# Kernel tuning notes

Hardware: AMD Instinct MI355X
Metric: run time of the kernel (lower is better)

## Reference

```python
import jax, jax.numpy as jnp
import numpy as np

B, T, D, DFF = 8, 2048, 1024, 4096
EPS = 1e-6
PLIF_ALPHA = 2.0


@jax.custom_vjp
def spike_fn(m):
    # hard threshold forward, atan surrogate backward (PLIF neuron)
    return (m > 0.0).astype(m.dtype)

def _spk_fwd(m):
    return (m > 0.0).astype(m.dtype), m

def _spk_bwd(m, g):
    ds = PLIF_ALPHA / (2.0 * (1.0 + (jnp.pi * 0.5 * PLIF_ALPHA * m) ** 2))
    return (g * ds,)

spike_fn.defvjp(_spk_fwd, _spk_bwd)


def _rmsnorm(x, w):
    rstd = jax.lax.rsqrt(jnp.mean(x * x, axis=-1, keepdims=True) + EPS)
    return x * rstd * w


def setup_inputs() -> dict:
    key = jax.random.key(0)
    ks = jax.random.split(key, 9)
    sc = 0.02
    return {
        'x': jax.random.normal(ks[0], (B, T, D), jnp.float32),
        'rms_w1': jnp.ones((D,), jnp.float32),
        'rms_w2': jnp.ones((D,), jnp.float32),
        'delta_w': sc * jax.random.normal(ks[1], (D, D), jnp.float32),
        'delta_b': jnp.zeros((D,), jnp.float32),
        'b_w': sc * jax.random.normal(ks[2], (D, D), jnp.float32),
        'b_b': jnp.zeros((D,), jnp.float32),
        'A_log': jnp.log(jnp.linspace(0.5, 2.0, D).astype(jnp.float32)),
        'log_tau': jnp.full((D,), jnp.log(2.0), jnp.float32),
        'plif_thr': jnp.ones((D,), jnp.float32),
        'syn_w': sc * jax.random.normal(ks[3], (D, D), jnp.float32),
        'syn_b': jnp.zeros((D,), jnp.float32),
        'gate_w': sc * jax.random.normal(ks[4], (D, D), jnp.float32),
        'gate_b': jnp.zeros((D,), jnp.float32),
        'ffn_g_w': sc * jax.random.normal(ks[5], (DFF, D), jnp.float32),
        'ffn_u_w': sc * jax.random.normal(ks[6], (DFF, D), jnp.float32),
        'ffn_d_w': sc * jax.random.normal(ks[7], (D, DFF), jnp.float32),
    }


def _forward(x, rms_w1, rms_w2, delta_w, delta_b, b_w, b_b, A_log, log_tau,
             plif_thr, syn_w, syn_b, gate_w, gate_b, ffn_g_w, ffn_u_w, ffn_d_w):
    Bx, Tx, Dx = x.shape
    # --- RMSNorm 1 ---
    y1 = _rmsnorm(x, rms_w1)
    # --- selective-scan style liquid inputs ---
    delta = jax.nn.softplus(jnp.einsum('btd,ed->bte', y1, delta_w) + delta_b)  # [B,T,D]
    bvec = delta * (jnp.einsum('btd,ed->bte', y1, b_w) + b_b)                  # [B,T,D]
    A = jnp.exp(-delta * jnp.exp(A_log))                                        # [B,T,D]

    # --- liquid recurrent scan: h_t = tanh(A_t * h_{t-1} + b_t) ---
    def liquid_step(h, ab):
        a_t, b_t = ab
        h = jnp.tanh(a_t * h + b_t)
        return h, h

    h0 = jnp.zeros((Bx, Dx), x.dtype)
    _, h_post = jax.lax.scan(liquid_step, h0,
                             (jnp.swapaxes(A, 0, 1), jnp.swapaxes(bvec, 0, 1)))
    h_post = jnp.swapaxes(h_post, 0, 1)  # [B,T,D]

    # --- PLIF spiking scan with soft reset ---
    pdec = jnp.exp(-1.0 / jnp.exp(log_tau))  # [D]

    def plif_step(v, h_t):
        v_pre = pdec * v + (1.0 - pdec) * h_t
        s = spike_fn(v_pre - plif_thr)
        return v_pre - s * plif_thr, s

    v0 = jnp.zeros((Bx, Dx), x.dtype)
    _, spike = jax.lax.scan(plif_step, v0, jnp.swapaxes(h_post, 0, 1))
    spike = jnp.swapaxes(spike, 0, 1)

    # --- SEW shortcut + synaptic gate ---
    spike_in = spike + h_post
    syn = jnp.einsum('btd,ed->bte', spike_in, syn_w) + syn_b
    gate = jax.nn.sigmoid(jnp.einsum('btd,ed->bte', spike_in, gate_w) + gate_b)
    x1 = x + syn * gate

    # --- RMSNorm 2 + SwiGLU FFN + residual ---
    y2 = _rmsnorm(x1, rms_w2)
    ffn_act = jax.nn.silu(y2 @ ffn_g_w.T) * (y2 @ ffn_u_w.T)
    return x1 + ffn_act @ ffn_d_w.T


def reference(x, rms_w1, rms_w2, delta_w, delta_b, b_w, b_b, A_log, log_tau,
              plif_thr, syn_w, syn_b, gate_w, gate_b, ffn_g_w, ffn_u_w, ffn_d_w):
    return _forward(x, rms_w1, rms_w2, delta_w, delta_b, b_w, b_b, A_log,
                    log_tau, plif_thr, syn_w, syn_b, gate_w, gate_b,
                    ffn_g_w, ffn_u_w, ffn_d_w)
```

## Files before the change

kernel.cpp:

```cpp
#include <hip/hip_runtime.h>
#include <stdint.h>

#define B_   8
#define T_   2048
#define D_   1024
#define DFF_ 4096
#define M_   (B_ * T_)

typedef __bf16 bf16;
typedef bf16  bf16x8 __attribute__((ext_vector_type(8)));
typedef bf16  bf16x4 __attribute__((ext_vector_type(4)));
typedef float f32x4  __attribute__((ext_vector_type(4)));

#define CAST_LDS(p) ((__attribute__((address_space(3))) void*)(p))
#define CAST_GLB(p) ((const __attribute__((address_space(1))) void*)(p))

struct CatArgs {
    const float* w1[3];
    const float* w2[3];
    bf16* dst[3];
    int end[3];
};

__global__ __launch_bounds__(256) void cvt_cat_kernel(CatArgs a) {
    const int b = blockIdx.x;
    const int seg = (b >= a.end[0] ? 1 : 0) + (b >= a.end[1] ? 1 : 0);
    const int d = b - (seg ? a.end[seg - 1] : 0);
    const int nt = d >> 8;
    const int r = d & 255;
    const float* src = ((r < 128) ? a.w1[seg] : a.w2[seg]) +
                       (size_t)((nt << 7) + (r & 127)) * D_;
    bf16* dst = a.dst[seg] + (size_t)d * D_;
    const int t = threadIdx.x;
    const float4 v = ((const float4*)src)[t];
    bf16x4 o;
    o[0] = (bf16)v.x; o[1] = (bf16)v.y; o[2] = (bf16)v.z; o[3] = (bf16)v.w;
    ((bf16x4*)dst)[t] = o;
}

__global__ __launch_bounds__(256) void cvt_plain_kernel(const float* __restrict__ s,
                                                        bf16* __restrict__ d) {
    const int i = (blockIdx.x * 256 + threadIdx.x) * 4;
    const float4 v = *(const float4*)(s + i);
    bf16x4 o;
    o[0] = (bf16)v.x; o[1] = (bf16)v.y; o[2] = (bf16)v.z; o[3] = (bf16)v.w;
    *(bf16x4*)(d + i) = o;
}

__global__ __launch_bounds__(256) void rmsnorm_kernel(const float* __restrict__ x,
                                                      const float* __restrict__ w,
                                                      bf16* __restrict__ y) {
    const size_t row = blockIdx.x;
    const int t = threadIdx.x;
    const float4 v = ((const float4*)(x + row * D_))[t];
    float ss = v.x * v.x + v.y * v.y + v.z * v.z + v.w * v.w;
#pragma unroll
    for (int off = 32; off; off >>= 1) ss += __shfl_down(ss, off);
    __shared__ float red[4];
    if ((t & 63) == 0) red[t >> 6] = ss;
    __syncthreads();
    const float total = red[0] + red[1] + red[2] + red[3];
    const float rstd = rsqrtf(total * (1.0f / (float)D_) + 1e-6f);
    const float4 wv = ((const float4*)w)[t];
    bf16x4 o;
    o[0] = (bf16)(v.x * rstd * wv.x);
    o[1] = (bf16)(v.y * rstd * wv.y);
    o[2] = (bf16)(v.z * rstd * wv.z);
    o[3] = (bf16)(v.w * rstd * wv.w);
    ((bf16x4*)(y + row * D_))[t] = o;
}

__global__ __launch_bounds__(256) void rmsnorm_bf_kernel(const bf16* __restrict__ x,
                                                         const float* __restrict__ w,
                                                         bf16* __restrict__ y) {
    const size_t row = blockIdx.x;
    const int t = threadIdx.x;
    const bf16x4 xv = ((const bf16x4*)(x + row * D_))[t];
    float f0 = (float)xv[0], f1 = (float)xv[1], f2 = (float)xv[2], f3 = (float)xv[3];
    float ss = f0 * f0 + f1 * f1 + f2 * f2 + f3 * f3;
#pragma unroll
    for (int off = 32; off; off >>= 1) ss += __shfl_down(ss, off);
    __shared__ float red[4];
    if ((t & 63) == 0) red[t >> 6] = ss;
    __syncthreads();
    const float total = red[0] + red[1] + red[2] + red[3];
    const float rstd = rsqrtf(total * (1.0f / (float)D_) + 1e-6f);
    const float4 wv = ((const float4*)w)[t];
    bf16x4 o;
    o[0] = (bf16)(f0 * rstd * wv.x);
    o[1] = (bf16)(f1 * rstd * wv.y);
    o[2] = (bf16)(f2 * rstd * wv.z);
    o[3] = (bf16)(f3 * rstd * wv.w);
    ((bf16x4*)(y + row * D_))[t] = o;
}

#define SCAN_C  32
#define SCAN_L  (T_ / SCAN_C)
#define SCAN_W  32
#define SCAN_PF 8

template <int N, int W0>
__device__ __forceinline__ void scan_body(const uint32_t* __restrict__ p,
                                          bf16* __restrict__ o, const int ts,
                                          const float pdec, const float om,
                                          const float th) {
    uint32_t buf[SCAN_PF];
#pragma unroll
    for (int i = 0; i < SCAN_PF; ++i) buf[i] = p[(size_t)i * D_];
    float h = 0.0f, v = 0.0f;
#pragma unroll 8
    for (int k = 0; k < N; ++k) {
        const uint32_t w = buf[k & (SCAN_PF - 1)];
        if (k + SCAN_PF < N) buf[k & (SCAN_PF - 1)] = p[(size_t)(k + SCAN_PF) * D_];
        const float a  = __builtin_bit_cast(float, w << 16);
        const float bb = __builtin_bit_cast(float, w & 0xffff0000u);
        const float xv = fmaf(a, h, bb);
        const float e2 = __expf(2.0f * xv);
        h = 1.0f - __fdividef(2.0f, 1.0f + e2);
        const float vpre = fmaf(pdec, v, om * h);
        const float s = (vpre > th) ? 1.0f : 0.0f;
        v = vpre - s * th;
        if (k >= W0) o[(size_t)(ts + k) * D_] = (bf16)(s + h);
    }
}

__global__ __launch_bounds__(256) void scan_kernel(const uint32_t* __restrict__ ABp,
                                                   const float* __restrict__ log_tau,
                                                   const float* __restrict__ thr,
                                                   bf16* __restrict__ sp) {
    const int g = blockIdx.x * 256 + threadIdx.x;
    const int d = g & (D_ - 1);
    const int bc = g >> 10;
    const int b = bc / SCAN_C;
    const int c = bc % SCAN_C;
    const float pdec = __expf(-__expf(-log_tau[d]));
    const float om = 1.0f - pdec;
    const float th = thr[d];
    const int t0 = c * SCAN_L;
    const uint32_t* base = ABp + (size_t)b * (T_ * D_) + d;
    bf16* o = sp + (size_t)b * (T_ * D_) + d;
    if (c == 0) {
        scan_body<SCAN_L, 0>(base, o, 0, pdec, om, th);
    } else {
        const int ts = t0 - SCAN_W;
        scan_body<SCAN_L + SCAN_W, SCAN_W>(base + (size_t)ts * D_, o, ts, pdec, om, th);
    }
}


#define STG_A(tt, kh)                                                                  \
  { bf16* l_ = lA0 + ((((tt) & 1) << 1) + (kh)) * 8192;                                \
    const bf16* g_ = gA + (tt) * 64 + ((kh) << 5);                                     \
    __builtin_amdgcn_global_load_lds(CAST_GLB(g_), CAST_LDS(l_), 16, 0, 0);            \
    __builtin_amdgcn_global_load_lds(CAST_GLB(g_ + g2), CAST_LDS(l_ + 4096), 16, 0, 0); }
#define STG_B(tt, kh)                                                                  \
  { bf16* l_ = lB0 + ((((tt) & 1) << 1) + (kh)) * 8192;                                \
    const bf16* g_ = gB + (tt) * 64 + ((kh) << 5);                                     \
    __builtin_amdgcn_global_load_lds(CAST_GLB(g_), CAST_LDS(l_), 16, 0, 0);            \
    __builtin_amdgcn_global_load_lds(CAST_GLB(g_ + g2), CAST_LDS(l_ + 4096), 16, 0, 0); }
#define DSREAD_A(KS, MH)                                                               \
  { const bf16* As_ = smA + (cb + (KS)) * 8192 + swz;                                  \
    _Pragma("unroll")                                                                  \
    for (int i = 0; i < 4; ++i)                                                        \
      af[i] = *(const bf16x8*)(As_ + (mr128 + (MH) * 64 + i * 16 + lane15) * 32);      \
  }
#define DSREAD_B(KS)                                                                   \
  { const bf16* Bs_ = smB + (cb + (KS)) * 8192 + swz;                                  \
    _Pragma("unroll")                                                                  \
    for (int j = 0; j < 4; ++j)                                                        \
      bfr[j] = *(const bf16x8*)(Bs_ + (nc64 + j * 16 + lane15) * 32);                  \
  }
#define MFMA16(MH)                                                                     \
  __builtin_amdgcn_s_setprio(1);                                                       \
  _Pragma("unroll")                                                                    \
  for (int i = 0; i < 4; ++i)                                                          \
    _Pragma("unroll")                                                                  \
    for (int j = 0; j < 4; ++j)                                                        \
      acc[(MH) * 4 + i][j] = __builtin_amdgcn_mfma_f32_16x16x32_bf16(                  \
          af[i], bfr[j], acc[(MH) * 4 + i][j], 0, 0, 0);                               \
  __builtin_amdgcn_s_setprio(0);
#define GBAR() __builtin_amdgcn_s_barrier()
#define LGKM0() asm volatile("s_waitcnt lgkmcnt(0)" ::: "memory")

template <int MODE>
__global__ __launch_bounds__(512, 2) void gemm8_kernel(
    const bf16* __restrict__ A, const bf16* __restrict__ Bw,
    const int Ncat, const int K, const int Nlog,
    const float* __restrict__ b1, const float* __restrict__ b2,
    const float* __restrict__ extra, const bf16* __restrict__ extra_bf,
    void* __restrict__ outp) {
    constexpr bool DUAL = (MODE != 3);
    __shared__ bf16 smem[65536] __attribute__((aligned(16)));
    bf16* const smA = smem;
    bf16* const smB = smem + 32768;

    const int tid = threadIdx.x;
    const int wave = tid >> 6;
    const int lane = tid & 63;
    const int lane15 = lane & 15;
    const int quad = lane >> 4;
    const int mr = wave >> 2;
    const int nc = wave & 3;
    const int mr128 = mr * 128;
    const int nc64 = nc * 64;
    const int swz = (quad ^ ((lane15 >> 1) & 3)) << 3;

    const int xcd = blockIdx.x & 7;
    const int c = blockIdx.x >> 3;
    const int mt = xcd * 8 + (c & 7);
    const int nt = (c >> 5) * 4 + ((c >> 3) & 3);

    const int srow = tid >> 2;
    const int scol = (((tid & 3) ^ ((srow >> 1) & 3)) << 3);
    const bf16* const gA = A + (size_t)(mt * 256 + srow) * K + scol;
    const bf16* const gB = Bw + (size_t)(nt * 256 + srow) * K + scol;
    const size_t g2 = (size_t)128 * K;
    bf16* const lA0 = smA + (wave << 9);
    bf16* const lB0 = smB + (wave << 9);

    const int NT = K >> 6;

    f32x4 acc[8][4] = {};
    bf16x8 af[4];
    bf16x8 bfr[4];

    STG_B(0, 0); STG_A(0, 0); STG_B(0, 1); STG_A(0, 1);
    asm volatile("s_waitcnt vmcnt(4)" ::: "memory");
    STG_B(1, 0); STG_A(1, 0); STG_B(1, 1);
    asm volatile("s_waitcnt vmcnt(6)" ::: "memory");
    GBAR();

    for (int t = 0; t < NT; ++t) {
        const int cb = (t & 1) << 1;

        DSREAD_A(0, 0); DSREAD_B(0);
        if (t + 1 < NT) STG_A(t + 1, 1);
        GBAR(); LGKM0();
        MFMA16(0);
        GBAR();

        DSREAD_A(0, 1);
        if (t + 2 < NT) STG_B(t + 2, 0);
        GBAR(); LGKM0();
        MFMA16(1);
        GBAR();

        DSREAD_A(1, 0); DSREAD_B(1);
        if (t + 2 < NT) STG_A(t + 2, 0);
        GBAR(); LGKM0();
        MFMA16(0);
        GBAR();

        DSREAD_A(1, 1);
        if (t + 2 < NT) {
            STG_B(t + 2, 1);
            asm volatile("s_waitcnt vmcnt(6)" ::: "memory");
        } else {
            asm volatile("s_waitcnt vmcnt(0)" ::: "memory");
        }
        GBAR(); LGKM0();
        MFMA16(1);
        GBAR();
    }

    if constexpr (DUAL) {
        float* const xch = (float*)smem;
        if (nc >= 2) {
            float* const dst = xch + (mr * 2 + (nc - 2)) * 8192;
#pragma unroll
            for (int i8 = 0; i8 < 8; ++i8)
#pragma unroll
                for (int j = 0; j < 4; ++j)
#pragma unroll
                    for (int r = 0; r < 4; ++r)
                        dst[(i8 * 16 + quad * 4 + r) * 64 + j * 16 + lane15] =
                            acc[i8][j][r];
        }
        __syncthreads();
        if (nc < 2) {
            const float* const src = xch + (mr * 2 + nc) * 8192;
            const int mbase = mt * 256 + mr128;
            const int nbase = nt * 128 + nc64;
#pragma unroll
            for (int i8 = 0; i8 < 8; ++i8)
#pragma unroll
                for (int j = 0; j < 4; ++j)
#pragma unroll
                    for (int r = 0; r < 4; ++r) {
                        const int rl = i8 * 16 + quad * 4 + r;
                        const int cl = j * 16 + lane15;
                        const int m = mbase + rl;
                        const int n = nbase + cl;
                        const size_t idx = (size_t)m * Nlog + n;
                        const float v1 = acc[i8][j][r];
                        const float v2 = src[rl * 64 + cl];
                        if constexpr (MODE == 0) {
                            const float dl = v1 + b1[n];
                            const float spv = (dl > 20.0f) ? dl : log1pf(__expf(dl));
                            const float bv = spv * (v2 + b2[n]);
                            const float av = __expf(-spv * __expf(extra[n]));
                            const uint32_t pa =
                                (uint32_t)__builtin_bit_cast(unsigned short, (bf16)av);
                            const uint32_t pb =
                                (uint32_t)__builtin_bit_cast(unsigned short, (bf16)bv);
                            ((uint32_t*)outp)[idx] = pa | (pb << 16);
                        } else if constexpr (MODE == 1) {
                            const float syn = v1 + b1[n];
                            const float z = v2 + b2[n];
                            const float gate = 1.0f / (1.0f + __expf(-z));
                            ((bf16*)outp)[idx] = (bf16)(extra[idx] + syn * gate);
                        } else {
                            const float sg = v1 / (1.0f + __expf(-v1));
                            ((bf16*)outp)[idx] = (bf16)(sg * v2);
                        }
                    }
        }
    } else {
        const int mbase = mt * 256 + mr128;
        const int nbase = nt * 256 + nc64;
#pragma unroll
        for (int i8 = 0; i8 < 8; ++i8)
#pragma unroll
            for (int j = 0; j < 4; ++j)
#pragma unroll
                for (int r = 0; r < 4; ++r) {
                    const int m = mbase + i8 * 16 + quad * 4 + r;
                    const int n = nbase + j * 16 + lane15;
                    const size_t idx = (size_t)m * Nlog + n;
                    ((float*)outp)[idx] = (float)extra_bf[idx] + acc[i8][j][r];
                }
    }
}

#undef STG_A
#undef STG_B
#undef DSREAD_A
#undef DSREAD_B
#undef MFMA16
#undef GBAR
#undef LGKM0

extern "C" void kernel_launch(void* const* d_in, const int* in_sizes, int n_in,
                              void* d_out, int out_size, void* d_ws, size_t ws_size,
                              hipStream_t stream) {
    const float* x        = (const float*)d_in[0];
    const float* rms_w1   = (const float*)d_in[1];
    const float* rms_w2   = (const float*)d_in[2];
    const float* delta_w  = (const float*)d_in[3];
    const float* delta_b  = (const float*)d_in[4];
    const float* b_w      = (const float*)d_in[5];
    const float* b_b      = (const float*)d_in[6];
    const float* A_log    = (const float*)d_in[7];
    const float* log_tau  = (const float*)d_in[8];
    const float* plif_thr = (const float*)d_in[9];
    const float* syn_w    = (const float*)d_in[10];
    const float* syn_b    = (const float*)d_in[11];
    const float* gate_w   = (const float*)d_in[12];
    const float* gate_b   = (const float*)d_in[13];
    const float* ffn_g_w  = (const float*)d_in[14];
    const float* ffn_u_w  = (const float*)d_in[15];
    const float* ffn_d_w  = (const float*)d_in[16];

    char* ws = (char*)d_ws;
    const size_t MB = 1024ull * 1024ull;
    bf16* wcat_db = (bf16*)(ws + 0 * MB);
    bf16* wcat_sg = (bf16*)(ws + 4 * MB);
    bf16* wcat_gu = (bf16*)(ws + 8 * MB);
    bf16* wd      = (bf16*)(ws + 24 * MB);
    bf16*     y1      = (bf16*)(ws + 32 * MB);
    uint32_t* ABp     = (uint32_t*)(ws + 64 * MB);
    bf16*     spikein = (bf16*)(ws + 128 * MB);
    bf16* x1 = (bf16*)(ws + 160 * MB);
    bf16* y2 = (bf16*)(ws + 224 * MB);
    bf16* act = (bf16*)(ws + 32 * MB);
    float* outF = (float*)d_out;

    CatArgs ca;
    ca.w1[0] = delta_w; ca.w2[0] = b_w;     ca.dst[0] = wcat_db;
    ca.w1[1] = syn_w;   ca.w2[1] = gate_w;  ca.dst[1] = wcat_sg;
    ca.w1[2] = ffn_g_w; ca.w2[2] = ffn_u_w; ca.dst[2] = wcat_gu;
    ca.end[0] = 2048; ca.end[1] = 4096; ca.end[2] = 12288;
    cvt_cat_kernel<<<12288, 256, 0, stream>>>(ca);
    cvt_plain_kernel<<<(D_ * DFF_) / 1024, 256, 0, stream>>>(ffn_d_w, wd);

    rmsnorm_kernel<<<M_, 256, 0, stream>>>(x, rms_w1, y1);

    gemm8_kernel<0><<<(2048 / 256) * (M_ / 256), 512, 0, stream>>>(
        y1, wcat_db, 2048, D_, D_, delta_b, b_b, A_log, nullptr, ABp);

    scan_kernel<<<(B_ * SCAN_C * D_) / 256, 256, 0, stream>>>(ABp, log_tau, plif_thr, spikein);

    gemm8_kernel<1><<<(2048 / 256) * (M_ / 256), 512, 0, stream>>>(
        spikein, wcat_sg, 2048, D_, D_, syn_b, gate_b, x, nullptr, x1);

    rmsnorm_bf_kernel<<<M_, 256, 0, stream>>>(x1, rms_w2, y2);

    gemm8_kernel<2><<<(8192 / 256) * (M_ / 256), 512, 0, stream>>>(
        y2, wcat_gu, 8192, D_, DFF_, nullptr, nullptr, nullptr, nullptr, act);

    gemm8_kernel<3><<<(1024 / 256) * (M_ / 256), 512, 0, stream>>>(
        act, wd, 1024, DFF_, D_, nullptr, nullptr, nullptr, x1, outF);
}
```

Baseline: 1.020 ms.

## Make GEMMs persistent over N tiles with 16-row weight interleaving

Every GEMM now launches a fixed grid of 256 blocks. Each block keeps one M tile and walks several N tiles in sequence, prefetching the next tile's B operand across tile boundaries so the load pipeline never drains. The concatenated weights are interleaved in 16-row groups, so each wave holds both halves of a dual GEMM (delta/b, syn/gate, gate/up) in its own accumulators. That removes the LDS exchange and the __syncthreads in the epilogue. The cost is fewer, longer blocks: load balance now depends on 256 blocks filling the CUs, and epilogue stores are no longer overlapped by other blocks' work.

```diff
diff --git a/kernel.cpp b/kernel.cpp
--- a/kernel.cpp
+++ b/kernel.cpp
@@ -22,14 +22,13 @@
     int end[3];
 };
 
-__global__ __launch_bounds__(256) void cvt_cat_kernel(CatArgs a) {
+__global__ __launch_bounds__(256) void cvt_cat16_kernel(CatArgs a) {
     const int b = blockIdx.x;
     const int seg = (b >= a.end[0] ? 1 : 0) + (b >= a.end[1] ? 1 : 0);
     const int d = b - (seg ? a.end[seg - 1] : 0);
-    const int nt = d >> 8;
-    const int r = d & 255;
-    const float* src = ((r < 128) ? a.w1[seg] : a.w2[seg]) +
-                       (size_t)((nt << 7) + (r & 127)) * D_;
+    const int rr = d & 31;
+    const float* src = ((rr < 16) ? a.w1[seg] : a.w2[seg]) +
+                       (size_t)(((d >> 5) << 4) + (d & 15)) * D_;
     bf16* dst = a.dst[seg] + (size_t)d * D_;
     const int t = threadIdx.x;
     const float4 v = ((const float4*)src)[t];
@@ -148,14 +147,14 @@
 }
 
 
-#define STG_A(tt, kh)                                                                  \
-  { bf16* l_ = lA0 + ((((tt) & 1) << 1) + (kh)) * 8192;                                \
-    const bf16* g_ = gA + (tt) * 64 + ((kh) << 5);                                     \
+#define STG_A(kt, par, kh)                                                             \
+  { bf16* l_ = lA0 + (((par) << 1) + (kh)) * 8192;                                     \
+    const bf16* g_ = gA + (kt) * 64 + ((kh) << 5);                                     \
     __builtin_amdgcn_global_load_lds(CAST_GLB(g_), CAST_LDS(l_), 16, 0, 0);            \
     __builtin_amdgcn_global_load_lds(CAST_GLB(g_ + g2), CAST_LDS(l_ + 4096), 16, 0, 0); }
-#define STG_B(tt, kh)                                                                  \
-  { bf16* l_ = lB0 + ((((tt) & 1) << 1) + (kh)) * 8192;                                \
-    const bf16* g_ = gB + (tt) * 64 + ((kh) << 5);                                     \
+#define STG_B(gb, kt, par, kh)                                                         \
+  { bf16* l_ = lB0 + (((par) << 1) + (kh)) * 8192;                                     \
+    const bf16* g_ = (gb) + (kt) * 64 + ((kh) << 5);                                   \
     __builtin_amdgcn_global_load_lds(CAST_GLB(g_), CAST_LDS(l_), 16, 0, 0);            \
     __builtin_amdgcn_global_load_lds(CAST_GLB(g_ + g2), CAST_LDS(l_ + 4096), 16, 0, 0); }
 #define DSREAD_A(KS, MH)                                                               \
@@ -183,13 +182,12 @@
 #define LGKM0() asm volatile("s_waitcnt lgkmcnt(0)" ::: "memory")
 
 template <int MODE>
-__global__ __launch_bounds__(512, 2) void gemm8_kernel(
+__global__ __launch_bounds__(512, 2) void gemm8p_kernel(
     const bf16* __restrict__ A, const bf16* __restrict__ Bw,
-    const int Ncat, const int K, const int Nlog,
+    const int K, const int Nlog, const int NTN,
     const float* __restrict__ b1, const float* __restrict__ b2,
     const float* __restrict__ extra, const bf16* __restrict__ extra_bf,
     void* __restrict__ outp) {
-    constexpr bool DUAL = (MODE != 3);
     __shared__ bf16 smem[65536] __attribute__((aligned(16)));
     bf16* const smA = smem;
     bf16* const smB = smem + 32768;
@@ -206,94 +204,89 @@
     const int swz = (quad ^ ((lane15 >> 1) & 3)) << 3;
 
     const int xcd = blockIdx.x & 7;
-    const int c = blockIdx.x >> 3;
-    const int mt = xcd * 8 + (c & 7);
-    const int nt = (c >> 5) * 4 + ((c >> 3) & 3);
+    const int cu  = blockIdx.x >> 3;
+    const int mt  = xcd * 8 + (cu & 7);
+    const int nt0 = cu >> 3;
+    const int TPB = NTN >> 2;
+    const int NT  = K >> 6;
+    const int S   = TPB * NT;
 
     const int srow = tid >> 2;
     const int scol = (((tid & 3) ^ ((srow >> 1) & 3)) << 3);
     const bf16* const gA = A + (size_t)(mt * 256 + srow) * K + scol;
-    const bf16* const gB = Bw + (size_t)(nt * 256 + srow) * K + scol;
     const size_t g2 = (size_t)128 * K;
+    const size_t dB = (size_t)1024 * K;
+    const bf16* gBc = Bw + (size_t)(nt0 * 256 + srow) * K + scol;
     bf16* const lA0 = smA + (wave << 9);
     bf16* const lB0 = smB + (wave << 9);
-
-    const int NT = K >> 6;
 
     f32x4 acc[8][4] = {};
     bf16x8 af[4];
     bf16x8 bfr[4];
 
-    STG_B(0, 0); STG_A(0, 0); STG_B(0, 1); STG_A(0, 1);
+    STG_B(gBc, 0, 0, 0); STG_A(0, 0, 0); STG_B(gBc, 0, 0, 1); STG_A(0, 0, 1);
     asm volatile("s_waitcnt vmcnt(4)" ::: "memory");
-    STG_B(1, 0); STG_A(1, 0); STG_B(1, 1);
+    STG_B(gBc, 1, 1, 0); STG_A(1, 1, 0); STG_B(gBc, 1, 1, 1);
     asm volatile("s_waitcnt vmcnt(6)" ::: "memory");
     GBAR();
 
-    for (int t = 0; t < NT; ++t) {
-        const int cb = (t & 1) << 1;
-
-        DSREAD_A(0, 0); DSREAD_B(0);
-        if (t + 1 < NT) STG_A(t + 1, 1);
-        GBAR(); LGKM0();
-        MFMA16(0);
-        GBAR();
-
-        DSREAD_A(0, 1);
-        if (t + 2 < NT) STG_B(t + 2, 0);
-        GBAR(); LGKM0();
-        MFMA16(1);
-        GBAR();
-
-        DSREAD_A(1, 0); DSREAD_B(1);
-        if (t + 2 < NT) STG_A(t + 2, 0);
-        GBAR(); LGKM0();
-        MFMA16(0);
-        GBAR();
-
-        DSREAD_A(1, 1);
-        if (t + 2 < NT) {
-            STG_B(t + 2, 1);
-            asm volatile("s_waitcnt vmcnt(6)" ::: "memory");
-        } else {
-            asm volatile("s_waitcnt vmcnt(0)" ::: "memory");
+    for (int w = 0; w < TPB; ++w) {
+        const bf16* const gBn = gBc + dB;
+        for (int t = 0; t < NT; ++t) {
+            const int s = w * NT + t;
+            const int cb = (t & 1) << 1;
+            const int tp1 = (t + 1 == NT) ? 0 : t + 1;
+            const int tp2 = (t + 2 >= NT) ? t + 2 - NT : t + 2;
+            const int par1 = (t + 1) & 1;
+            const int par2 = t & 1;
+            const bf16* const gB2 = (t + 2 >= NT) ? gBn : gBc;
+            const bool st1 = (s + 1 < S);
+            const bool st2 = (s + 2 < S);
+
+            DSREAD_A(0, 0); DSREAD_B(0);
+            if (st1) STG_A(tp1, par1, 1);
+            GBAR(); LGKM0();
+            MFMA16(0);
+            GBAR();
+
+            DSREAD_A(0, 1);
+            if (st2) STG_B(gB2, tp2, par2, 0);
+            GBAR(); LGKM0();
+            MFMA16(1);
+            GBAR();
+
+            DSREAD_A(1, 0); DSREAD_B(1);
+            if (st2) STG_A(tp2, par2, 0);
+            GBAR(); LGKM0();
+            MFMA16(0);
+            GBAR();
+
+            DSREAD_A(1, 1);
+            if (st2) {
+                STG_B(gB2, tp2, par2, 1);
+                asm volatile("s_waitcnt vmcnt(6)" ::: "memory");
+            } else {
+                asm volatile("s_waitcnt vmcnt(0)" ::: "memory");
+            }
+            GBAR(); LGKM0();
+            MFMA16(1);
+            GBAR();
         }
-        GBAR(); LGKM0();
-        MFMA16(1);
-        GBAR();
-    }
-
-    if constexpr (DUAL) {
-        float* const xch = (float*)smem;
-        if (nc >= 2) {
-            float* const dst = xch + (mr * 2 + (nc - 2)) * 8192;
+
+        if constexpr (MODE != 3) {
+            const int nlog0 = (nt0 + w * 4) * 128 + nc * 32;
+            const int mbase = mt * 256 + mr128;
 #pragma unroll
             for (int i8 = 0; i8 < 8; ++i8)
 #pragma unroll
-                for (int j = 0; j < 4; ++j)
-#pragma unroll
-                    for (int r = 0; r < 4; ++r)
-                        dst[(i8 * 16 + quad * 4 + r) * 64 + j * 16 + lane15] =
-                            acc[i8][j][r];
-        }
-        __syncthreads();
-        if (nc < 2) {
-            const float* const src = xch + (mr * 2 + nc) * 8192;
-            const int mbase = mt * 256 + mr128;
-            const int nbase = nt * 128 + nc64;
-#pragma unroll
-            for (int i8 = 0; i8 < 8; ++i8)
-#pragma unroll
-                for (int j = 0; j < 4; ++j)
+                for (int jp = 0; jp < 2; ++jp)
 #pragma unroll
                     for (int r = 0; r < 4; ++r) {
-                        const int rl = i8 * 16 + quad * 4 + r;
-                        const int cl = j * 16 + lane15;
-                        const int m = mbase + rl;
-                        const int n = nbase + cl;
+                        const int m = mbase + i8 * 16 + quad * 4 + r;
+                        const int n = nlog0 + jp * 16 + lane15;
                         const size_t idx = (size_t)m * Nlog + n;
-                        const float v1 = acc[i8][j][r];
-                        const float v2 = src[rl * 64 + cl];
+                        const float v1 = acc[i8][jp * 2][r];
+                        const float v2 = acc[i8][jp * 2 + 1][r];
                         if constexpr (MODE == 0) {
                             const float dl = v1 + b1[n];
                             const float spv = (dl > 20.0f) ? dl : log1pf(__expf(dl));
@@ -314,21 +307,30 @@
                             ((bf16*)outp)[idx] = (bf16)(sg * v2);
                         }
                     }
+        } else {
+            const int mbase = mt * 256 + mr128;
+            const int nbase = (nt0 + w * 4) * 256 + nc64;
+#pragma unroll
+            for (int i8 = 0; i8 < 8; ++i8)
+#pragma unroll
+                for (int j = 0; j < 4; ++j)
+#pragma unroll
+                    for (int r = 0; r < 4; ++r) {
+                        const int m = mbase + i8 * 16 + quad * 4 + r;
+                        const int n = nbase + j * 16 + lane15;
+                        const size_t idx = (size_t)m * Nlog + n;
+                        ((float*)outp)[idx] = (float)extra_bf[idx] + acc[i8][j][r];
+                    }
         }
-    } else {
-        const int mbase = mt * 256 + mr128;
-        const int nbase = nt * 256 + nc64;
-#pragma unroll
-        for (int i8 = 0; i8 < 8; ++i8)
-#pragma unroll
-            for (int j = 0; j < 4; ++j)
-#pragma unroll
-                for (int r = 0; r < 4; ++r) {
-                    const int m = mbase + i8 * 16 + quad * 4 + r;
-                    const int n = nbase + j * 16 + lane15;
-                    const size_t idx = (size_t)m * Nlog + n;
-                    ((float*)outp)[idx] = (float)extra_bf[idx] + acc[i8][j][r];
-                }
+
+        if (w + 1 < TPB) {
+#pragma unroll
+            for (int i8 = 0; i8 < 8; ++i8)
+#pragma unroll
+                for (int j = 0; j < 4; ++j)
+                    acc[i8][j] = (f32x4){0.0f, 0.0f, 0.0f, 0.0f};
+            gBc = gBn;
+        }
     }
 }
 
@@ -380,24 +382,24 @@
     ca.w1[1] = syn_w;   ca.w2[1] = gate_w;  ca.dst[1] = wcat_sg;
     ca.w1[2] = ffn_g_w; ca.w2[2] = ffn_u_w; ca.dst[2] = wcat_gu;
     ca.end[0] = 2048; ca.end[1] = 4096; ca.end[2] = 12288;
-    cvt_cat_kernel<<<12288, 256, 0, stream>>>(ca);
+    cvt_cat16_kernel<<<12288, 256, 0, stream>>>(ca);
     cvt_plain_kernel<<<(D_ * DFF_) / 1024, 256, 0, stream>>>(ffn_d_w, wd);
 
     rmsnorm_kernel<<<M_, 256, 0, stream>>>(x, rms_w1, y1);
 
-    gemm8_kernel<0><<<(2048 / 256) * (M_ / 256), 512, 0, stream>>>(
-        y1, wcat_db, 2048, D_, D_, delta_b, b_b, A_log, nullptr, ABp);
+    gemm8p_kernel<0><<<256, 512, 0, stream>>>(
+        y1, wcat_db, D_, D_, 8, delta_b, b_b, A_log, nullptr, ABp);
 
     scan_kernel<<<(B_ * SCAN_C * D_) / 256, 256, 0, stream>>>(ABp, log_tau, plif_thr, spikein);
 
-    gemm8_kernel<1><<<(2048 / 256) * (M_ / 256), 512, 0, stream>>>(
-        spikein, wcat_sg, 2048, D_, D_, syn_b, gate_b, x, nullptr, x1);
+    gemm8p_kernel<1><<<256, 512, 0, stream>>>(
+        spikein, wcat_sg, D_, D_, 8, syn_b, gate_b, x, nullptr, x1);
 
     rmsnorm_bf_kernel<<<M_, 256, 0, stream>>>(x1, rms_w2, y2);
 
-    gemm8_kernel<2><<<(8192 / 256) * (M_ / 256), 512, 0, stream>>>(
-        y2, wcat_gu, 8192, D_, DFF_, nullptr, nullptr, nullptr, nullptr, act);
-
-    gemm8_kernel<3><<<(1024 / 256) * (M_ / 256), 512, 0, stream>>>(
-        act, wd, 1024, DFF_, D_, nullptr, nullptr, nullptr, x1, outF);
-}
+    gemm8p_kernel<2><<<256, 512, 0, stream>>>(
+        y2, wcat_gu, D_, DFF_, 32, nullptr, nullptr, nullptr, nullptr, act);
+
+    gemm8p_kernel<3><<<256, 512, 0, stream>>>(
+        act, wd, DFF_, D_, 4, nullptr, nullptr, nullptr, x1, outF);
+}
```

Result: faster. 883.6 us (-13.4%).
